# Kernel optimization log

Measured on AMD Instinct MI355X. Metric: run time of the kernel, lower is better.

Reference implementation:

```python
import jax, jax.numpy as jnp
import numpy as np

H, W, D, HEADS = 32, 32, 16, 8
EPS = 1e-5

def _ln(x, g, b):
    m = jnp.mean(x, -1, keepdims=True)
    v = jnp.mean((x - m) ** 2, -1, keepdims=True)
    return (x - m) / jnp.sqrt(v + EPS) * g + b

def _attn(x, w_qkv, w_proj, b_proj):
    # x: (Bb, N, C); torch Linear: y = x @ W.T + b
    Bb, N, C = x.shape
    hd = C // HEADS
    qkv = jnp.einsum('bnc,dc->bnd', x, w_qkv).reshape(Bb, N, 3, HEADS, hd)
    q, k, v = qkv[:, :, 0], qkv[:, :, 1], qkv[:, :, 2]  # (Bb,N,h,hd)
    att = jnp.einsum('bnhd,bmhd->bhnm', q, k) * (hd ** -0.5)
    att = jax.nn.softmax(att, axis=-1)
    o = jnp.einsum('bhnm,bmhd->bnhd', att, v).reshape(Bb, N, C)
    return jnp.einsum('bnc,dc->bnd', o, w_proj) + b_proj

def setup_inputs() -> dict:
    key = jax.random.key(0)
    ks = jax.random.split(key, 8)
    C, HID = 96, 384
    s = 0.02
    return {
        'x': jax.random.normal(ks[0], (1, C, D, H, W), jnp.float32),
        'norm1_g': jnp.ones((C,), jnp.float32),
        'norm1_b': jnp.zeros((C,), jnp.float32),
        'qkv_hw_w': jax.random.normal(ks[1], (3 * C, C), jnp.float32) * s,
        'proj_hw_w': jax.random.normal(ks[2], (C, C), jnp.float32) * s,
        'proj_hw_b': jnp.zeros((C,), jnp.float32),
        'qkv_t_w': jax.random.normal(ks[3], (3 * C, C), jnp.float32) * s,
        'proj_t_w': jax.random.normal(ks[4], (C, C), jnp.float32) * s,
        'proj_t_b': jnp.zeros((C,), jnp.float32),
        'norm2_g': jnp.ones((C,), jnp.float32),
        'norm2_b': jnp.zeros((C,), jnp.float32),
        'fc1_w': jax.random.normal(ks[5], (HID, C), jnp.float32) * s,
        'fc1_b': jnp.zeros((HID,), jnp.float32),
        'fc2_w': jax.random.normal(ks[6], (C, HID), jnp.float32) * s,
        'fc2_b': jnp.zeros((C,), jnp.float32),
    }

def reference(x, norm1_g, norm1_b, qkv_hw_w, proj_hw_w, proj_hw_b,
              qkv_t_w, proj_t_w, proj_t_b, norm2_g, norm2_b,
              fc1_w, fc1_b, fc2_w, fc2_b):
    B, C = x.shape[0], x.shape[1]
    HWn = H * W
    xf = x.reshape(B, C, -1).transpose(0, 2, 1)  # (B, L, C), L = D*H*W (D-major)
    shortcut = xf
    n1 = _ln(xf, norm1_g, norm1_b).reshape(B, D, HWn, C)
    # attention over H*W tokens (batched over B*D)
    a_hw = _attn(n1.reshape(B * D, HWn, C), qkv_hw_w, proj_hw_w, proj_hw_b)
    a_hw = a_hw.reshape(B, -1, C)  # D-major token order
    # attention over D tokens (batched over B*H*W)
    a_t = _attn(n1.transpose(0, 2, 1, 3).reshape(B * HWn, D, C), qkv_t_w, proj_t_w, proj_t_b)
    a_t = a_t.reshape(B, HWn * D, C)  # HW-major order (faithful to original view)
    out_res = shortcut + a_hw + a_t
    h1 = jax.nn.gelu(jnp.einsum('blc,hc->blh', _ln(out_res, norm2_g, norm2_b), fc1_w) + fc1_b,
                     approximate=False)
    mlp_out = jnp.einsum('blh,ch->blc', h1, fc2_w) + fc2_b
    out_ffn = out_res + mlp_out
    out = out_ffn.reshape(B, H, W, D, C).transpose(0, 4, 3, 1, 2)  # (B,C,D,H,W)
    return out
```

## Files before the change

kernel.cpp:

```cpp
#include <hip/hip_runtime.h>
#include <math.h>

#define L_TOK 16384
#define C_DIM 96
#define N_HEADS 8
#define HD 12
#define D_DIM 16
#define HW_N 1024
#define HID_DIM 384
#define SCALE 0.2886751345948129f
#define LOG2E 1.4426950408889634f

typedef _Float16 h4 __attribute__((ext_vector_type(4)));
typedef __fp16 fp16x2 __attribute__((ext_vector_type(2)));
typedef float v4f __attribute__((ext_vector_type(4)));

static __device__ __forceinline__ float fast_exp2(float x) {
#if __has_builtin(__builtin_amdgcn_exp2f)
    return __builtin_amdgcn_exp2f(x);
#else
    float r;
    asm("v_exp_f32 %0, %1" : "=v"(r) : "v"(x));
    return r;
#endif
}

static __device__ __forceinline__ h4 pack4(float a, float b, float c, float d) {
    fp16x2 lo = __builtin_amdgcn_cvt_pkrtz(a, b);
    fp16x2 hi = __builtin_amdgcn_cvt_pkrtz(c, d);
    union { fp16x2 p[2]; h4 v; } u;
    u.p[0] = lo; u.p[1] = hi;
    return u.v;
}

__global__ __launch_bounds__(256) void prep_kernel(
    const float* __restrict__ x, const float* __restrict__ g1,
    const float* __restrict__ b1, _Float16* __restrict__ n1h,
    const float* __restrict__ qkv_hw_w, const float* __restrict__ qkv_t_w,
    const float* __restrict__ proj_hw_w, const float* __restrict__ proj_t_w,
    const float* __restrict__ proj_hw_b, const float* __restrict__ proj_t_b,
    const float* __restrict__ fc1_w, const float* __restrict__ fc2_w,
    _Float16* __restrict__ wq, _Float16* __restrict__ wp,
    _Float16* __restrict__ wf1, _Float16* __restrict__ wf2,
    float* __restrict__ bp) {
    if (blockIdx.x < 64) {
        int l = blockIdx.x * 256 + threadIdx.x;
        float v[C_DIM];
        float s = 0.f;
#pragma unroll
        for (int c = 0; c < C_DIM; c++) {
            v[c] = x[(size_t)c * L_TOK + l];
            s += v[c];
        }
        float mean = s * (1.f / C_DIM);
        float var = 0.f;
#pragma unroll
        for (int c = 0; c < C_DIM; c++) {
            float dd = v[c] - mean;
            var += dd * dd;
        }
        float r = rsqrtf(var * (1.f / C_DIM) + 1e-5f);
        _Float16* op = n1h + (size_t)l * C_DIM;
#pragma unroll
        for (int c = 0; c < C_DIM; c += 4) {
            h4 o;
            o[0] = (_Float16)((v[c + 0] - mean) * r * g1[c + 0] + b1[c + 0]);
            o[1] = (_Float16)((v[c + 1] - mean) * r * g1[c + 1] + b1[c + 1]);
            o[2] = (_Float16)((v[c + 2] - mean) * r * g1[c + 2] + b1[c + 2]);
            o[3] = (_Float16)((v[c + 3] - mean) * r * g1[c + 3] + b1[c + 3]);
            *(h4*)(op + c) = o;
        }
        return;
    }
    int idx = (blockIdx.x - 64) * 256 + threadIdx.x;
    if (idx < 55296) {
        int n = idx / 96;
        float v = (n < 288) ? qkv_hw_w[idx] : qkv_t_w[idx - 27648];
        bool isq = (n < 96) || (n >= 288 && n < 384);
        wq[idx] = (_Float16)(isq ? v * (SCALE * LOG2E) : v);
    } else if (idx < 55296 + 18432) {
        int i = idx - 55296;
        int n = i / 192, k = i % 192;
        float v = (k < 96) ? proj_hw_w[n * 96 + k] : proj_t_w[n * 96 + k - 96];
        wp[i] = (_Float16)v;
    } else if (idx < 73728 + 36864) {
        int i = idx - 73728;
        wf1[i] = (_Float16)fc1_w[i];
    } else if (idx < 110592 + 36864) {
        int i = idx - 110592;
        wf2[i] = (_Float16)fc2_w[i];
    } else if (idx < 147456 + 96) {
        int i = idx - 147456;
        bp[i] = proj_hw_b[i] + proj_t_b[i];
    }
}

#define GBM 64
#define GBN 48
#define GBK 96
#define LSTRIDE 104

__global__ __launch_bounds__(256) void gemm_qkv(
    const _Float16* __restrict__ A, const _Float16* __restrict__ W,
    _Float16* __restrict__ Qp, _Float16* __restrict__ Kp,
    _Float16* __restrict__ VTp, _Float16* __restrict__ Tp) {
    __shared__ _Float16 As[GBM][LSTRIDE];
    __shared__ _Float16 Ws[GBN][LSTRIDE];
    const int t = threadIdx.x;
    const int m0 = blockIdx.x * GBM;
    const int n0 = blockIdx.y * GBN;
    const int lane = t & 63, w = t >> 6, g = lane >> 4, r = lane & 15;

    v4f acc[3];
#pragma unroll
    for (int nt = 0; nt < 3; nt++) {
        acc[nt][0] = 0.f; acc[nt][1] = 0.f; acc[nt][2] = 0.f; acc[nt][3] = 0.f;
    }
#pragma unroll
    for (int i = 0; i < 3; i++) {
        int idx = t + i * 256;
        int row = idx / 12, c = idx % 12;
        *(float4*)&As[row][c * 8] =
            *(const float4*)&A[(size_t)(m0 + row) * 96 + c * 8];
    }
#pragma unroll
    for (int i = 0; i < 3; i++) {
        int idx = t + i * 256;
        if (idx < 576) {
            int row = idx / 12, c = idx % 12;
            *(float4*)&Ws[row][c * 8] =
                *(const float4*)&W[(size_t)(n0 + row) * 96 + c * 8];
        }
    }
    __syncthreads();
#pragma unroll
    for (int ks = 0; ks < 6; ks++) {
        h4 af = *(const h4*)&As[w * 16 + r][ks * 16 + 4 * g];
#pragma unroll
        for (int nt = 0; nt < 3; nt++) {
            h4 wf = *(const h4*)&Ws[nt * 16 + r][ks * 16 + 4 * g];
            acc[nt] = __builtin_amdgcn_mfma_f32_16x16x16f16(wf, af, acc[nt], 0, 0, 0);
        }
    }

    const int m = m0 + w * 16 + r;
    const int d = m >> 10, hw = m & 1023;
    const int by = blockIdx.y;
#pragma unroll
    for (int nt = 0; nt < 3; nt++) {
        const int nb = n0 + nt * 16 + 4 * g;
        h4 ov;
        ov[0] = (_Float16)acc[nt][0]; ov[1] = (_Float16)acc[nt][1];
        ov[2] = (_Float16)acc[nt][2]; ov[3] = (_Float16)acc[nt][3];
        if (by < 2) {
            int n = nb;
            int h = (unsigned)n / 12u, dd = n - h * 12;
            *(h4*)&Qp[((size_t)(d * 8 + h) * 1024 + hw) * 12 + dd] = ov;
        } else if (by < 4) {
            int n = nb - 96;
            int h = (unsigned)n / 12u, dd = n - h * 12;
            *(h4*)&Kp[((size_t)(d * 8 + h) * 1024 + hw) * 12 + dd] = ov;
        } else if (by < 6) {
            int n = nb - 192;
            int h = (unsigned)n / 12u, dd = n - h * 12;
#pragma unroll
            for (int j = 0; j < 4; j++) {
                VTp[((size_t)(d * 8 + h) * 12 + dd + j) * 1024 + hw] = ov[j];
            }
        } else {
            *(h4*)&Tp[(size_t)(hw * 16 + d) * 288 + (nb - 288)] = ov;
        }
    }
}

#define WSTRIDE 104

#define STAGE(buf, src, stride)                                              \
    {                                                                        \
        _Pragma("unroll")                                                    \
        for (int i_ = 0; i_ < 5; i_++) {                                     \
            int idx_ = t + i_ * 256;                                         \
            if (idx_ < 1152) {                                               \
                int row_ = idx_ / 12, c_ = idx_ % 12;                        \
                *(float4*)&Wb[buf][row_ * WSTRIDE + c_ * 8] =                \
                    *(const float4*)&(src)[(size_t)row_ * (stride) + c_ * 8];\
            }                                                                \
        }                                                                    \
    }

#define PROJ_CHUNK(buf, kc)                                                  \
    {                                                                        \
        _Pragma("unroll")                                                    \
        for (int ks = 0; ks < 6; ks++) {                                     \
            _Pragma("unroll")                                                \
            for (int nt = 0; nt < 6; nt++) {                                 \
                h4 wf = *(const h4*)&Wb[buf][(nt * 16 + r) * WSTRIDE +       \
                                             ks * 16 + 4 * g];               \
                acc[nt] = __builtin_amdgcn_mfma_f32_16x16x16f16(             \
                    wf, afp[kc][ks], acc[nt], 0, 0, 0);                      \
            }                                                                \
        }                                                                    \
    }

#define FC1_CHUNK(buf, nc)                                                   \
    {                                                                        \
        v4f f[6];                                                            \
        _Pragma("unroll")                                                    \
        for (int nt = 0; nt < 6; nt++) {                                     \
            f[nt][0] = 0.f; f[nt][1] = 0.f; f[nt][2] = 0.f; f[nt][3] = 0.f;  \
        }                                                                    \
        _Pragma("unroll")                                                    \
        for (int ks = 0; ks < 6; ks++) {                                     \
            _Pragma("unroll")                                                \
            for (int nt = 0; nt < 6; nt++) {                                 \
                h4 wf = *(const h4*)&Wb[buf][(nt * 16 + r) * WSTRIDE +       \
                                             ks * 16 + 4 * g];               \
                f[nt] = __builtin_amdgcn_mfma_f32_16x16x16f16(               \
                    wf, n2f[ks], f[nt], 0, 0, 0);                            \
            }                                                                \
        }                                                                    \
        _Pragma("unroll")                                                    \
        for (int nt = 0; nt < 6; nt++) {                                     \
            const int nb = (nc) * 96 + nt * 16 + 4 * g;                      \
            float4 bv = *(const float4*)&f1b[nb];                            \
            float u0 = f[nt][0] + bv.x, u1 = f[nt][1] + bv.y;                \
            float u2 = f[nt][2] + bv.z, u3 = f[nt][3] + bv.w;                \
            hf[nc][nt] =                                                     \
                pack4(0.5f * u0 * (1.f + erff(u0 * 0.7071067811865476f)),    \
                      0.5f * u1 * (1.f + erff(u1 * 0.7071067811865476f)),    \
                      0.5f * u2 * (1.f + erff(u2 * 0.7071067811865476f)),    \
                      0.5f * u3 * (1.f + erff(u3 * 0.7071067811865476f)));   \
        }                                                                    \
    }

#define FC2_CHUNK(buf, kc)                                                   \
    {                                                                        \
        _Pragma("unroll")                                                    \
        for (int ks = 0; ks < 6; ks++) {                                     \
            _Pragma("unroll")                                                \
            for (int nt = 0; nt < 6; nt++) {                                 \
                h4 wf = *(const h4*)&Wb[buf][(nt * 16 + r) * WSTRIDE +       \
                                             ks * 16 + 4 * g];               \
                o6[nt] = __builtin_amdgcn_mfma_f32_16x16x16f16(              \
                    wf, hf[kc][ks], o6[nt], 0, 0, 0);                        \
            }                                                                \
        }                                                                    \
    }

__global__ __launch_bounds__(256) void fused_mlp(
    const _Float16* __restrict__ A, const _Float16* __restrict__ wp,
    const float* __restrict__ bp, const float* __restrict__ x,
    const float* __restrict__ g2, const float* __restrict__ b2,
    const _Float16* __restrict__ wf1, const float* __restrict__ f1b,
    const _Float16* __restrict__ wf2, const float* __restrict__ f2b,
    float* __restrict__ out) {
    __shared__ _Float16 Wb[2][96 * WSTRIDE];
    __shared__ float sh[96 * 68];

    const int t = threadIdx.x;
    const int bx = blockIdx.x;
    const int bxs = (bx & 7) * 32 + (bx >> 3);
    const int m0 = bxs * 64;
    const int lane = t & 63, w = t >> 6, g = lane >> 4, r = lane & 15;
    const int ml = w * 16 + r;
    const int m = m0 + ml;

    h4 afp[2][6];
#pragma unroll
    for (int kc = 0; kc < 2; kc++)
#pragma unroll
        for (int ks = 0; ks < 6; ks++)
            afp[kc][ks] =
                *(const h4*)&A[(size_t)m * 192 + kc * 96 + ks * 16 + 4 * g];
    float xr[24];
#pragma unroll
    for (int nt = 0; nt < 6; nt++) {
#pragma unroll
        for (int j = 0; j < 4; j++)
            xr[nt * 4 + j] = x[(size_t)(nt * 16 + 4 * g + j) * L_TOK + m];
    }

    STAGE(0, wp, 192);
    __syncthreads();
    STAGE(1, wp + 96, 192);
    v4f acc[6];
#pragma unroll
    for (int nt = 0; nt < 6; nt++) {
        acc[nt][0] = 0.f; acc[nt][1] = 0.f; acc[nt][2] = 0.f; acc[nt][3] = 0.f;
    }
    PROJ_CHUNK(0, 0);
    __syncthreads();
    STAGE(0, wf1, 96);
    PROJ_CHUNK(1, 1);
    float v[24];
    float sum = 0.f;
#pragma unroll
    for (int nt = 0; nt < 6; nt++) {
        const int nb = nt * 16 + 4 * g;
        float4 bv = *(const float4*)&bp[nb];
        float a0 = acc[nt][0] + bv.x + xr[nt * 4 + 0];
        float a1 = acc[nt][1] + bv.y + xr[nt * 4 + 1];
        float a2 = acc[nt][2] + bv.z + xr[nt * 4 + 2];
        float a3 = acc[nt][3] + bv.w + xr[nt * 4 + 3];
        v[nt * 4 + 0] = a0; v[nt * 4 + 1] = a1;
        v[nt * 4 + 2] = a2; v[nt * 4 + 3] = a3;
        sum += (a0 + a1) + (a2 + a3);
    }
    sum += __shfl_xor(sum, 16, 64);
    sum += __shfl_xor(sum, 32, 64);
    float mean = sum * (1.f / 96.f);
    float ss = 0.f;
#pragma unroll
    for (int i = 0; i < 24; i++) {
        float dd = v[i] - mean;
        ss += dd * dd;
    }
    ss += __shfl_xor(ss, 16, 64);
    ss += __shfl_xor(ss, 32, 64);
    float rstd = rsqrtf(ss * (1.f / 96.f) + 1e-5f);
    h4 n2f[6];
#pragma unroll
    for (int nt = 0; nt < 6; nt++) {
        const int nb = nt * 16 + 4 * g;
        float4 gg = *(const float4*)&g2[nb];
        float4 bb = *(const float4*)&b2[nb];
        n2f[nt] = pack4((v[nt * 4 + 0] - mean) * rstd * gg.x + bb.x,
                        (v[nt * 4 + 1] - mean) * rstd * gg.y + bb.y,
                        (v[nt * 4 + 2] - mean) * rstd * gg.z + bb.z,
                        (v[nt * 4 + 3] - mean) * rstd * gg.w + bb.w);
    }
    __syncthreads();
    h4 hf[4][6];
    STAGE(1, wf1 + 96 * 96, 96);
    FC1_CHUNK(0, 0);
    __syncthreads();
    STAGE(0, wf1 + 2 * 96 * 96, 96);
    FC1_CHUNK(1, 1);
    __syncthreads();
    STAGE(1, wf1 + 3 * 96 * 96, 96);
    FC1_CHUNK(0, 2);
    __syncthreads();
    STAGE(0, wf2, 384);
    FC1_CHUNK(1, 3);
    __syncthreads();
    v4f o6[6];
#pragma unroll
    for (int nt = 0; nt < 6; nt++) {
        o6[nt][0] = 0.f; o6[nt][1] = 0.f; o6[nt][2] = 0.f; o6[nt][3] = 0.f;
    }
    STAGE(1, wf2 + 96, 384);
    FC2_CHUNK(0, 0);
    __syncthreads();
    STAGE(0, wf2 + 192, 384);
    FC2_CHUNK(1, 1);
    __syncthreads();
    STAGE(1, wf2 + 288, 384);
    FC2_CHUNK(0, 2);
    __syncthreads();
    FC2_CHUNK(1, 3);

#pragma unroll
    for (int nt = 0; nt < 6; nt++) {
        const int nb = nt * 16 + 4 * g;
        float4 bv = *(const float4*)&f2b[nb];
        sh[(nb + 0) * 68 + ml] = o6[nt][0] + bv.x + v[nt * 4 + 0];
        sh[(nb + 1) * 68 + ml] = o6[nt][1] + bv.y + v[nt * 4 + 1];
        sh[(nb + 2) * 68 + ml] = o6[nt][2] + bv.z + v[nt * 4 + 2];
        sh[(nb + 3) * 68 + ml] = o6[nt][3] + bv.w + v[nt * 4 + 3];
    }
    __syncthreads();
    const int hh = m0 >> 9, ww0 = (m0 >> 4) & 31;
#pragma unroll
    for (int i = 0; i < 6; i++) {
        int task = t + i * 256;
        int n = task >> 4, dd = task & 15;
        float4 ov;
        ov.x = sh[n * 68 + dd];
        ov.y = sh[n * 68 + dd + 16];
        ov.z = sh[n * 68 + dd + 32];
        ov.w = sh[n * 68 + dd + 48];
        *(float4*)&out[(size_t)n * L_TOK + dd * 1024 + hh * 32 + ww0] = ov;
    }
}

__global__ __launch_bounds__(256) void attn_hw_kernel(
    const _Float16* __restrict__ Qp, const _Float16* __restrict__ Kp,
    const _Float16* __restrict__ VTp, _Float16* __restrict__ o_cat) {
    __shared__ _Float16 K_lds[1024 * 12];
    __shared__ _Float16 VT_lds[13 * 1032];
    const int t = threadIdx.x;
    const int sliceid = blockIdx.x;
    const int qb = blockIdx.y;
    const int d = sliceid >> 3, h = sliceid & 7;
    const size_t tokbase = (size_t)d * HW_N;
    const int hoff = h * HD;
    const size_t slice = (size_t)sliceid;

    {
        const float4* Kg = (const float4*)(Kp + slice * 12288);
        float4* K4 = (float4*)K_lds;
#pragma unroll
        for (int i = 0; i < 6; i++) K4[t + i * 256] = Kg[t + i * 256];
        const float4* Vg = (const float4*)(VTp + slice * 12288);
#pragma unroll
        for (int i = 0; i < 6; i++) {
            int off = t + i * 256;
            int row = off >> 7, col = (off & 127) * 8;
            *(float4*)&VT_lds[row * 1032 + col] = Vg[off];
        }
        unsigned* zp = (unsigned*)&VT_lds[12 * 1032];
        zp[t] = 0x3C003C00u; zp[t + 256] = 0x3C003C00u;
        if (t < 4) zp[t + 512] = 0x3C003C00u;
    }

    const int lane = t & 63, w = t >> 6, g = lane >> 4, r = lane & 15;
    const int q0w = qb * 128 + w * 32;

    h4 zf; zf[0] = zf[1] = zf[2] = zf[3] = (_Float16)0.f;
    h4 qf[2];
    {
        const _Float16* Qbase = Qp + (slice * 1024 + q0w + r) * 12 + 4 * g;
#pragma unroll
        for (int qt = 0; qt < 2; qt++) {
            qf[qt] = (g < 3) ? *(const h4*)(Qbase + qt * 16 * 12) : zf;
        }
    }

    v4f acc[2];
#pragma unroll
    for (int qt = 0; qt < 2; qt++) {
        acc[qt][0] = acc[qt][1] = acc[qt][2] = acc[qt][3] = 0.f;
    }

    const int koff = r * 12 + 4 * g;
    const int rowc = (r < 12) ? r : 12;
    const int voff = rowc * 1032 + 4 * g;

    __syncthreads();

    v4f zero; zero[0] = zero[1] = zero[2] = zero[3] = 0.f;
#pragma unroll 4
    for (int kt = 0; kt < HW_N / 16; kt++) {
        h4 kf = (g < 3) ? *(const h4*)&K_lds[kt * 192 + koff] : zf;
        h4 vf = *(const h4*)&VT_lds[voff + kt * 16];
#pragma unroll
        for (int qt = 0; qt < 2; qt++) {
            v4f s = __builtin_amdgcn_mfma_f32_16x16x16f16(kf, qf[qt], zero, 0, 0, 0);
            h4 pf = pack4(fast_exp2(s[0]), fast_exp2(s[1]),
                          fast_exp2(s[2]), fast_exp2(s[3]));
            acc[qt] = __builtin_amdgcn_mfma_f32_16x16x16f16(vf, pf, acc[qt], 0, 0, 0);
        }
    }

#pragma unroll
    for (int qt = 0; qt < 2; qt++) {
        float denom = __shfl(acc[qt][0], 48 + r, 64);
        float rs = 1.f / denom;
        if (g < 3) {
            _Float16* op =
                o_cat + (tokbase + q0w + qt * 16 + r) * 192 + hoff + 4 * g;
            h4 o;
            o[0] = (_Float16)(acc[qt][0] * rs);
            o[1] = (_Float16)(acc[qt][1] * rs);
            o[2] = (_Float16)(acc[qt][2] * rs);
            o[3] = (_Float16)(acc[qt][3] * rs);
            *(h4*)op = o;
        }
    }
}

__global__ __launch_bounds__(256) void attn_t_kernel(
    const _Float16* __restrict__ Tp, _Float16* __restrict__ o_cat) {
    int gid = blockIdx.x * 256 + threadIdx.x;
    int hw = gid >> 7;
    int h = (gid >> 4) & 7;
    int q = gid & 15;
    const int hoff = h * HD;
    const _Float16* base = Tp + (size_t)(hw * 16) * 288;

    float qr[HD];
    {
        const _Float16* p = base + q * 288 + hoff;
        h4 a = *(const h4*)p, b = *(const h4*)(p + 4), c = *(const h4*)(p + 8);
#pragma unroll
        for (int e = 0; e < 4; e++) {
            qr[e] = (float)a[e]; qr[4 + e] = (float)b[e]; qr[8 + e] = (float)c[e];
        }
    }
    float s[D_DIM];
    float mx = -1e30f;
#pragma unroll
    for (int j = 0; j < D_DIM; j++) {
        const _Float16* kp = base + j * 288 + 96 + hoff;
        h4 a = *(const h4*)kp, b = *(const h4*)(kp + 4), c = *(const h4*)(kp + 8);
        float dot = 0.f;
#pragma unroll
        for (int e = 0; e < 4; e++) {
            dot += qr[e] * (float)a[e] + qr[4 + e] * (float)b[e] +
                   qr[8 + e] * (float)c[e];
        }
        s[j] = dot;
        mx = fmaxf(mx, dot);
    }
    float sum = 0.f;
#pragma unroll
    for (int j = 0; j < D_DIM; j++) {
        s[j] = fast_exp2(s[j] - mx);
        sum += s[j];
    }
    float rs = 1.f / sum;
    float o[HD];
#pragma unroll
    for (int e = 0; e < HD; e++) o[e] = 0.f;
#pragma unroll
    for (int j = 0; j < D_DIM; j++) {
        const _Float16* vp = base + j * 288 + 192 + hoff;
        h4 a = *(const h4*)vp, b = *(const h4*)(vp + 4), c = *(const h4*)(vp + 8);
        float p = s[j];
#pragma unroll
        for (int e = 0; e < 4; e++) {
            o[e] += p * (float)a[e];
            o[4 + e] += p * (float)b[e];
            o[8 + e] += p * (float)c[e];
        }
    }
    _Float16* op = o_cat + ((size_t)hw * D_DIM + q) * 192 + 96 + hoff;
#pragma unroll
    for (int e = 0; e < HD; e += 4) {
        h4 a;
        a[0] = (_Float16)(o[e] * rs); a[1] = (_Float16)(o[e + 1] * rs);
        a[2] = (_Float16)(o[e + 2] * rs); a[3] = (_Float16)(o[e + 3] * rs);
        *(h4*)(op + e) = a;
    }
}

extern "C" void kernel_launch(void* const* d_in, const int* in_sizes, int n_in,
                              void* d_out, int out_size, void* d_ws,
                              size_t ws_size, hipStream_t stream) {
    const float* x         = (const float*)d_in[0];
    const float* norm1_g   = (const float*)d_in[1];
    const float* norm1_b   = (const float*)d_in[2];
    const float* qkv_hw_w  = (const float*)d_in[3];
    const float* proj_hw_w = (const float*)d_in[4];
    const float* proj_hw_b = (const float*)d_in[5];
    const float* qkv_t_w   = (const float*)d_in[6];
    const float* proj_t_w  = (const float*)d_in[7];
    const float* proj_t_b  = (const float*)d_in[8];
    const float* norm2_g   = (const float*)d_in[9];
    const float* norm2_b   = (const float*)d_in[10];
    const float* fc1_w     = (const float*)d_in[11];
    const float* fc1_b     = (const float*)d_in[12];
    const float* fc2_w     = (const float*)d_in[13];
    const float* fc2_b     = (const float*)d_in[14];
    float* out = (float*)d_out;

    char* ws = (char*)d_ws;
    _Float16* n1h    = (_Float16*)ws;
    _Float16* o_cat  = n1h + (size_t)L_TOK * C_DIM;
    float*    out_res= (float*)(o_cat + (size_t)L_TOK * 192);
    _Float16* packs  = (_Float16*)(out_res + (size_t)L_TOK * C_DIM);
    _Float16* Qp     = packs;
    _Float16* Kp     = Qp + 1572864;
    _Float16* VTp    = Kp + 1572864;
    _Float16* Tp     = VTp + 1572864;
    _Float16* wq     = Tp + (size_t)L_TOK * 288;
    _Float16* wp     = wq + 55296;
    _Float16* wf1    = wp + 18432;
    _Float16* wf2    = wf1 + 36864;
    float*    bp     = (float*)(wf2 + 36864);

    prep_kernel<<<641, 256, 0, stream>>>(x, norm1_g, norm1_b, n1h,
                                         qkv_hw_w, qkv_t_w, proj_hw_w,
                                         proj_t_w, proj_hw_b, proj_t_b,
                                         fc1_w, fc2_w, wq, wp, wf1, wf2, bp);
    gemm_qkv<<<dim3(L_TOK / GBM, 576 / GBN), 256, 0, stream>>>(
        n1h, wq, Qp, Kp, VTp, Tp);
    attn_hw_kernel<<<dim3(128, 8), 256, 0, stream>>>(Qp, Kp, VTp, o_cat);
    attn_t_kernel<<<(HW_N * N_HEADS * D_DIM) / 256, 256, 0, stream>>>(Tp, o_cat);
    fused_mlp<<<L_TOK / 64, 256, 0, stream>>>(
        o_cat, wp, bp, x, norm2_g, norm2_b, wf1, fc1_b, wf2, fc2_b, out);
}
```

Measured before the change: 90.31 us.

## Split fused MLP tiles across waves by N to double block count

The fused MLP kernel now handles 32 tokens per block instead of 64, and each pair of waves splits the output columns in half. The grid doubles to 512 blocks. LayerNorm statistics become a single-pass sum and sum-of-squares reduced through shared memory, and normalized activations are shared through LDS. FC2 partial sums from the two column-halves are combined in shared memory. The aim is better CU occupancy and fewer registers per thread, at the cost of extra syncs, reloading weights per smaller tile, and narrower float2 stores.

Measured after the change: 87.62 us, median of 2. -3.0%, faster.

```diff
diff --git a/kernel.cpp b/kernel.cpp
--- a/kernel.cpp
+++ b/kernel.cpp
@@ -193,9 +193,9 @@
         _Pragma("unroll")                                                    \
         for (int ks = 0; ks < 6; ks++) {                                     \
             _Pragma("unroll")                                                \
-            for (int nt = 0; nt < 6; nt++) {                                 \
-                h4 wf = *(const h4*)&Wb[buf][(nt * 16 + r) * WSTRIDE +       \
-                                             ks * 16 + 4 * g];               \
+            for (int nt = 0; nt < 3; nt++) {                                 \
+                h4 wf = *(const h4*)&Wb[buf][(ni * 48 + nt * 16 + r) *       \
+                                             WSTRIDE + ks * 16 + 4 * g];     \
                 acc[nt] = __builtin_amdgcn_mfma_f32_16x16x16f16(             \
                     wf, afp[kc][ks], acc[nt], 0, 0, 0);                      \
             }                                                                \
@@ -204,24 +204,26 @@
 
 #define FC1_CHUNK(buf, nc)                                                   \
     {                                                                        \
-        v4f f[6];                                                            \
+        v4f f[3];                                                            \
         _Pragma("unroll")                                                    \
-        for (int nt = 0; nt < 6; nt++) {                                     \
+        for (int nt = 0; nt < 3; nt++) {                                     \
             f[nt][0] = 0.f; f[nt][1] = 0.f; f[nt][2] = 0.f; f[nt][3] = 0.f;  \
         }                                                                    \
         _Pragma("unroll")                                                    \
         for (int ks = 0; ks < 6; ks++) {                                     \
+            h4 af = *(const h4*)&n2_lds[(mi * 16 + r) * WSTRIDE +            \
+                                        ks * 16 + 4 * g];                    \
             _Pragma("unroll")                                                \
-            for (int nt = 0; nt < 6; nt++) {                                 \
-                h4 wf = *(const h4*)&Wb[buf][(nt * 16 + r) * WSTRIDE +       \
-                                             ks * 16 + 4 * g];               \
+            for (int nt = 0; nt < 3; nt++) {                                 \
+                h4 wf = *(const h4*)&Wb[buf][(ni * 48 + nt * 16 + r) *       \
+                                             WSTRIDE + ks * 16 + 4 * g];     \
                 f[nt] = __builtin_amdgcn_mfma_f32_16x16x16f16(               \
-                    wf, n2f[ks], f[nt], 0, 0, 0);                            \
+                    wf, af, f[nt], 0, 0, 0);                                 \
             }                                                                \
         }                                                                    \
         _Pragma("unroll")                                                    \
-        for (int nt = 0; nt < 6; nt++) {                                     \
-            const int nb = (nc) * 96 + nt * 16 + 4 * g;                      \
+        for (int nt = 0; nt < 3; nt++) {                                     \
+            const int nb = (nc) * 96 + ni * 48 + nt * 16 + 4 * g;            \
             float4 bv = *(const float4*)&f1b[nb];                            \
             float u0 = f[nt][0] + bv.x, u1 = f[nt][1] + bv.y;                \
             float u2 = f[nt][2] + bv.z, u3 = f[nt][3] + bv.w;                \
@@ -236,11 +238,11 @@
 #define FC2_CHUNK(buf, kc)                                                   \
     {                                                                        \
         _Pragma("unroll")                                                    \
-        for (int ks = 0; ks < 6; ks++) {                                     \
+        for (int ks = 0; ks < 3; ks++) {                                     \
             _Pragma("unroll")                                                \
             for (int nt = 0; nt < 6; nt++) {                                 \
                 h4 wf = *(const h4*)&Wb[buf][(nt * 16 + r) * WSTRIDE +       \
-                                             ks * 16 + 4 * g];               \
+                                             ni * 48 + ks * 16 + 4 * g];     \
                 o6[nt] = __builtin_amdgcn_mfma_f32_16x16x16f16(              \
                     wf, hf[kc][ks], o6[nt], 0, 0, 0);                        \
             }                                                                \
@@ -255,15 +257,18 @@
     const _Float16* __restrict__ wf2, const float* __restrict__ f2b,
     float* __restrict__ out) {
     __shared__ _Float16 Wb[2][96 * WSTRIDE];
-    __shared__ float sh[96 * 68];
+    __shared__ _Float16 n2_lds[32 * WSTRIDE];
+    __shared__ float sh[96 * 34];
+    __shared__ float red[2][32][2];
 
     const int t = threadIdx.x;
     const int bx = blockIdx.x;
-    const int bxs = (bx & 7) * 32 + (bx >> 3);
-    const int m0 = bxs * 64;
+    const int bxs = (bx & 7) * 64 + (bx >> 3);
+    const int m0 = bxs * 32;
     const int lane = t & 63, w = t >> 6, g = lane >> 4, r = lane & 15;
-    const int ml = w * 16 + r;
-    const int m = m0 + ml;
+    const int mi = w >> 1, ni = w & 1;
+    const int rl = mi * 16 + r;
+    const int m = m0 + rl;
 
     h4 afp[2][6];
 #pragma unroll
@@ -272,66 +277,69 @@
         for (int ks = 0; ks < 6; ks++)
             afp[kc][ks] =
                 *(const h4*)&A[(size_t)m * 192 + kc * 96 + ks * 16 + 4 * g];
-    float xr[24];
-#pragma unroll
-    for (int nt = 0; nt < 6; nt++) {
+    float xr[12];
+#pragma unroll
+    for (int nt = 0; nt < 3; nt++) {
 #pragma unroll
         for (int j = 0; j < 4; j++)
-            xr[nt * 4 + j] = x[(size_t)(nt * 16 + 4 * g + j) * L_TOK + m];
+            xr[nt * 4 + j] =
+                x[(size_t)(ni * 48 + nt * 16 + 4 * g + j) * L_TOK + m];
     }
 
     STAGE(0, wp, 192);
     __syncthreads();
     STAGE(1, wp + 96, 192);
-    v4f acc[6];
-#pragma unroll
-    for (int nt = 0; nt < 6; nt++) {
+    v4f acc[3];
+#pragma unroll
+    for (int nt = 0; nt < 3; nt++) {
         acc[nt][0] = 0.f; acc[nt][1] = 0.f; acc[nt][2] = 0.f; acc[nt][3] = 0.f;
     }
     PROJ_CHUNK(0, 0);
     __syncthreads();
     STAGE(0, wf1, 96);
     PROJ_CHUNK(1, 1);
-    float v[24];
-    float sum = 0.f;
-#pragma unroll
-    for (int nt = 0; nt < 6; nt++) {
-        const int nb = nt * 16 + 4 * g;
-        float4 bv = *(const float4*)&bp[nb];
+    float v[12];
+    float s1 = 0.f, s2 = 0.f;
+#pragma unroll
+    for (int nt = 0; nt < 3; nt++) {
+        const int c = ni * 48 + nt * 16 + 4 * g;
+        float4 bv = *(const float4*)&bp[c];
         float a0 = acc[nt][0] + bv.x + xr[nt * 4 + 0];
         float a1 = acc[nt][1] + bv.y + xr[nt * 4 + 1];
         float a2 = acc[nt][2] + bv.z + xr[nt * 4 + 2];
         float a3 = acc[nt][3] + bv.w + xr[nt * 4 + 3];
         v[nt * 4 + 0] = a0; v[nt * 4 + 1] = a1;
         v[nt * 4 + 2] = a2; v[nt * 4 + 3] = a3;
-        sum += (a0 + a1) + (a2 + a3);
-    }
-    sum += __shfl_xor(sum, 16, 64);
-    sum += __shfl_xor(sum, 32, 64);
-    float mean = sum * (1.f / 96.f);
-    float ss = 0.f;
-#pragma unroll
-    for (int i = 0; i < 24; i++) {
-        float dd = v[i] - mean;
-        ss += dd * dd;
-    }
-    ss += __shfl_xor(ss, 16, 64);
-    ss += __shfl_xor(ss, 32, 64);
-    float rstd = rsqrtf(ss * (1.f / 96.f) + 1e-5f);
-    h4 n2f[6];
-#pragma unroll
-    for (int nt = 0; nt < 6; nt++) {
-        const int nb = nt * 16 + 4 * g;
-        float4 gg = *(const float4*)&g2[nb];
-        float4 bb = *(const float4*)&b2[nb];
-        n2f[nt] = pack4((v[nt * 4 + 0] - mean) * rstd * gg.x + bb.x,
-                        (v[nt * 4 + 1] - mean) * rstd * gg.y + bb.y,
-                        (v[nt * 4 + 2] - mean) * rstd * gg.z + bb.z,
-                        (v[nt * 4 + 3] - mean) * rstd * gg.w + bb.w);
-    }
-    __syncthreads();
-    h4 hf[4][6];
+        s1 += (a0 + a1) + (a2 + a3);
+        s2 += (a0 * a0 + a1 * a1) + (a2 * a2 + a3 * a3);
+    }
+    s1 += __shfl_xor(s1, 16, 64);
+    s1 += __shfl_xor(s1, 32, 64);
+    s2 += __shfl_xor(s2, 16, 64);
+    s2 += __shfl_xor(s2, 32, 64);
+    if (g == 0) { red[ni][rl][0] = s1; red[ni][rl][1] = s2; }
+    __syncthreads();
+    {
+        float t1 = red[0][rl][0] + red[1][rl][0];
+        float t2 = red[0][rl][1] + red[1][rl][1];
+        float mean = t1 * (1.f / 96.f);
+        float var = t2 * (1.f / 96.f) - mean * mean;
+        float rstd = rsqrtf(var + 1e-5f);
+#pragma unroll
+        for (int nt = 0; nt < 3; nt++) {
+            const int c = ni * 48 + nt * 16 + 4 * g;
+            float4 gg = *(const float4*)&g2[c];
+            float4 bb = *(const float4*)&b2[c];
+            h4 o = pack4((v[nt * 4 + 0] - mean) * rstd * gg.x + bb.x,
+                         (v[nt * 4 + 1] - mean) * rstd * gg.y + bb.y,
+                         (v[nt * 4 + 2] - mean) * rstd * gg.z + bb.z,
+                         (v[nt * 4 + 3] - mean) * rstd * gg.w + bb.w);
+            *(h4*)&n2_lds[rl * WSTRIDE + c] = o;
+        }
+    }
     STAGE(1, wf1 + 96 * 96, 96);
+    __syncthreads();
+    h4 hf[4][3];
     FC1_CHUNK(0, 0);
     __syncthreads();
     STAGE(0, wf1 + 2 * 96 * 96, 96);
@@ -358,15 +366,32 @@
     FC2_CHUNK(0, 2);
     __syncthreads();
     FC2_CHUNK(1, 3);
-
-#pragma unroll
-    for (int nt = 0; nt < 6; nt++) {
-        const int nb = nt * 16 + 4 * g;
-        float4 bv = *(const float4*)&f2b[nb];
-        sh[(nb + 0) * 68 + ml] = o6[nt][0] + bv.x + v[nt * 4 + 0];
-        sh[(nb + 1) * 68 + ml] = o6[nt][1] + bv.y + v[nt * 4 + 1];
-        sh[(nb + 2) * 68 + ml] = o6[nt][2] + bv.z + v[nt * 4 + 2];
-        sh[(nb + 3) * 68 + ml] = o6[nt][3] + bv.w + v[nt * 4 + 3];
+    __syncthreads();
+
+    if (ni == 0) {
+#pragma unroll
+        for (int nt = 0; nt < 6; nt++) {
+#pragma unroll
+            for (int j = 0; j < 4; j++) {
+                const int c = nt * 16 + 4 * g + j;
+                float val = o6[nt][j] + f2b[c];
+                if (nt < 3) val += v[nt * 4 + j];
+                sh[c * 34 + rl] = val;
+            }
+        }
+    }
+    __syncthreads();
+    if (ni == 1) {
+#pragma unroll
+        for (int nt = 0; nt < 6; nt++) {
+#pragma unroll
+            for (int j = 0; j < 4; j++) {
+                const int c = nt * 16 + 4 * g + j;
+                float val = o6[nt][j];
+                if (nt >= 3) val += v[(nt - 3) * 4 + j];
+                sh[c * 34 + rl] += val;
+            }
+        }
     }
     __syncthreads();
     const int hh = m0 >> 9, ww0 = (m0 >> 4) & 31;
@@ -374,12 +399,10 @@
     for (int i = 0; i < 6; i++) {
         int task = t + i * 256;
         int n = task >> 4, dd = task & 15;
-        float4 ov;
-        ov.x = sh[n * 68 + dd];
-        ov.y = sh[n * 68 + dd + 16];
-        ov.z = sh[n * 68 + dd + 32];
-        ov.w = sh[n * 68 + dd + 48];
-        *(float4*)&out[(size_t)n * L_TOK + dd * 1024 + hh * 32 + ww0] = ov;
+        float2 ov;
+        ov.x = sh[n * 34 + dd];
+        ov.y = sh[n * 34 + 16 + dd];
+        *(float2*)&out[(size_t)n * L_TOK + dd * 1024 + hh * 32 + ww0] = ov;
     }
 }
 
@@ -577,6 +600,6 @@
         n1h, wq, Qp, Kp, VTp, Tp);
     attn_hw_kernel<<<dim3(128, 8), 256, 0, stream>>>(Qp, Kp, VTp, o_cat);
     attn_t_kernel<<<(HW_N * N_HEADS * D_DIM) / 256, 256, 0, stream>>>(Tp, o_cat);
-    fused_mlp<<<L_TOK / 64, 256, 0, stream>>>(
+    fused_mlp<<<512, 256, 0, stream>>>(
         o_cat, wp, bp, x, norm2_g, norm2_b, wf1, fc1_b, wf2, fc2_b, out);
 }
```
